# Kernel tuning notes

Hardware: AMD Instinct MI355X
Metric: run time of the kernel (lower is better)

The kernel has to match this reference:

```python
import jax, jax.numpy as jnp
from jax import lax
import numpy as np

K = 48          # dim_embedding_key
PAST = 20
FUT = 40
N = 65536       # total surrounding-agent nodes
E = 1048576     # edges
B = 1           # batch (structurally forced to 1 by the original code)


def conv1d_relu(x, w, b):
    # x: [B, 2, T], w: [K, 2, 3], padding=1 -> relu(Conv1d)
    y = lax.conv_general_dilated(x, w, (1,), ((1, 1),),
                                 dimension_numbers=('NCH', 'OIH', 'NCH'))
    return jax.nn.relu(y + b[None, :, None])


def gru_cell(xt, h, Wih, Whh, bih, bhh):
    gi = xt @ Wih.T + bih
    gh = h @ Whh.T + bhh
    ir, iz, inn = jnp.split(gi, 3, axis=-1)
    hr, hz, hn = jnp.split(gh, 3, axis=-1)
    r = jax.nn.sigmoid(ir + hr)
    z = jax.nn.sigmoid(iz + hz)
    n = jnp.tanh(inn + r * hn)
    return (1 - z) * n + z * h


def gru_last(x, Wih, Whh, bih, bhh):
    # x: [Nb, T, Din]; returns final hidden state [Nb, H] (torch GRU, h0 = 0)
    h0 = jnp.zeros((x.shape[0], Whh.shape[1]), x.dtype)
    def step(h, xt):
        h2 = gru_cell(xt, h, Wih, Whh, bih, bhh)
        return h2, None
    hT, _ = lax.scan(step, h0, jnp.swapaxes(x, 0, 1))
    return hT


def gcn_conv(x, row, col, w, W, b, n):
    # PyG GCNConv(normalize=True): add self loops (weight 1), symmetric norm,
    # x @ W.T, gather at source `row`, scatter-add at target `col`, + bias.
    loop = jnp.arange(n)
    row = jnp.concatenate([row, loop])
    col = jnp.concatenate([col, loop])
    w = jnp.concatenate([w, jnp.ones((n,), w.dtype)])
    deg = jax.ops.segment_sum(w, col, num_segments=n)
    dinv = jnp.where(deg > 0, lax.rsqrt(jnp.where(deg > 0, deg, 1.0)), 0.0)
    norm = dinv[row] * w * dinv[col]
    xw = x @ W.T
    msg = xw[row] * norm[:, None]
    return jax.ops.segment_sum(msg, col, num_segments=n) + b


def forward(past, future, x, edge_index, edge_weight,
            conv_past_w, conv_past_b, conv_fut_w, conv_fut_b,
            enc_past_Wih, enc_past_Whh, enc_past_bih, enc_past_bhh,
            enc_fut_Wih, enc_fut_Whh, enc_fut_bih, enc_fut_bhh,
            dec_Wih, dec_Whh, dec_bih, dec_bhh,
            fc_w, fc_b, gcn1_w, gcn1_b, gcn2_w, gcn2_b):
    present0 = past[:, -1, :2]                                  # [B, 2]

    # --- surrounding agents: conv1d + GRU encoder over all N nodes ---
    inter_past = jnp.swapaxes(x.reshape(-1, PAST, 2), 1, 2)     # [N, 2, T]
    story_embed = jnp.swapaxes(conv1d_relu(inter_past, conv_past_w, conv_past_b), 1, 2)
    state_past = gru_last(story_embed, enc_past_Wih, enc_past_Whh, enc_past_bih, enc_past_bhh)  # [N, K]

    # --- GCN interaction (edge_weight nonempty branch); dropout is eval-mode identity ---
    ei = edge_index.reshape(2, -1)
    ew = edge_weight.reshape(-1)
    x1 = jax.nn.relu(gcn_conv(state_past, ei[0], ei[1], ew, gcn1_w, gcn1_b, N))
    x1 = gcn_conv(x1, ei[0], ei[1], ew, gcn2_w, gcn2_b, N)
    interact_past = x1[0].reshape(B, -1)                        # [B, K] (B == 1)

    # --- ego past / future encoders ---
    past_embed = jnp.swapaxes(conv1d_relu(jnp.swapaxes(past, 1, 2), conv_past_w, conv_past_b), 1, 2)
    fut_embed = jnp.swapaxes(conv1d_relu(jnp.swapaxes(future, 1, 2), conv_fut_w, conv_fut_b), 1, 2)
    target_past = gru_last(past_embed, enc_past_Wih, enc_past_Whh, enc_past_bih, enc_past_bhh)   # [B, K]
    state_fut = gru_last(fut_embed, enc_fut_Wih, enc_fut_Whh, enc_fut_bih, enc_fut_bhh)          # [B, K]

    state_conc = jnp.concatenate([interact_past, target_past, state_fut], axis=-1)               # [B, 3K]

    zeros_in = jnp.zeros_like(state_conc)
    def step(carry, i):
        h, present = carry
        inp = jnp.where(i == 0, state_conc, zeros_in)
        h = gru_cell(inp, h, dec_Wih, dec_Whh, dec_bih, dec_bhh)
        coords = present + h @ fc_w.T + fc_b
        return (h, coords), coords
    (_, _), coords_seq = lax.scan(step, (jnp.zeros((B, 3 * K), past.dtype), present0), jnp.arange(FUT))
    return jnp.swapaxes(coords_seq, 0, 1)                        # [B, FUT, 2]


def setup_inputs() -> dict:
    ks = jax.random.split(jax.random.key(0), 32)
    def p(k, shape, s=0.1):
        return jax.random.normal(k, shape, jnp.float32) * s
    inp = {
        'past': p(ks[0], (B, PAST, 2), 1.0),
        'future': p(ks[1], (B, FUT, 2), 1.0),
        'x': p(ks[2], (N, PAST, 2), 1.0),
        'edge_index': jax.random.randint(ks[3], (1, 2, E), 0, N, jnp.int32),
        'edge_weight': jax.random.uniform(ks[4], (1, E), jnp.float32),
        'conv_past_w': p(ks[5], (K, 2, 3)), 'conv_past_b': p(ks[6], (K,)),
        'conv_fut_w': p(ks[7], (K, 2, 3)), 'conv_fut_b': p(ks[8], (K,)),
        'enc_past_Wih': p(ks[9], (3 * K, K)), 'enc_past_Whh': p(ks[10], (3 * K, K)),
        'enc_past_bih': p(ks[11], (3 * K,)), 'enc_past_bhh': p(ks[12], (3 * K,)),
        'enc_fut_Wih': p(ks[13], (3 * K, K)), 'enc_fut_Whh': p(ks[14], (3 * K, K)),
        'enc_fut_bih': p(ks[15], (3 * K,)), 'enc_fut_bhh': p(ks[16], (3 * K,)),
        'dec_Wih': p(ks[17], (9 * K, 3 * K)), 'dec_Whh': p(ks[18], (9 * K, 3 * K)),
        'dec_bih': p(ks[19], (9 * K,)), 'dec_bhh': p(ks[20], (9 * K,)),
        'fc_w': p(ks[21], (2, 3 * K)), 'fc_b': p(ks[22], (2,)),
        'gcn1_w': p(ks[23], (K, K)), 'gcn1_b': p(ks[24], (K,)),
        'gcn2_w': p(ks[25], (K, K)), 'gcn2_b': p(ks[26], (K,)),
    }
    return inp


def reference(past, future, x, edge_index, edge_weight,
              conv_past_w, conv_past_b, conv_fut_w, conv_fut_b,
              enc_past_Wih, enc_past_Whh, enc_past_bih, enc_past_bhh,
              enc_fut_Wih, enc_fut_Whh, enc_fut_bih, enc_fut_bhh,
              dec_Wih, dec_Whh, dec_bih, dec_bhh,
              fc_w, fc_b, gcn1_w, gcn1_b, gcn2_w, gcn2_b):
    return forward(past, future, x, edge_index, edge_weight,
                   conv_past_w, conv_past_b, conv_fut_w, conv_fut_b,
                   enc_past_Wih, enc_past_Whh, enc_past_bih, enc_past_bhh,
                   enc_fut_Wih, enc_fut_Whh, enc_fut_bih, enc_fut_bhh,
                   dec_Wih, dec_Whh, dec_bih, dec_bhh,
                   fc_w, fc_b, gcn1_w, gcn1_b, gcn2_w, gcn2_b)
```

## Files before the change

kernel.cpp:

```cpp
#include <hip/hip_runtime.h>
#include <math.h>

#define NN 65536
#define NE 1048576
#define KH 48
#define G3 144
#define DEGB 512

#define CAP_L1 8192
#define CAP_S1 4096
#define CAP_E2 65536
#define CAP_S2 8192

#define OFF_MARK1  0u
#define OFF_MARK2  262144u
#define OFF_CNT    524288u
#define OFF_L1R    524352u
#define OFF_L1W    557120u
#define OFF_S1G    589888u
#define OFF_E2R    606272u
#define OFF_E2S    868416u
#define OFF_E2W    1130560u
#define OFF_S2     1392704u
#define OFF_DEG2   1425472u
#define OFF_STATE  1458240u
#define OFF_X1     3031104u
#define OFF_TPSF   3817536u
#define OFF_WHH16  3818048u
#define OFF_GI0P   3942464u

typedef _Float16 h2_t __attribute__((ext_vector_type(2)));
typedef _Float16 h4_t __attribute__((ext_vector_type(4)));

__device__ __forceinline__ float sigmf(float x) { return 1.0f / (1.0f + expf(-x)); }

#if __has_builtin(__builtin_amdgcn_fdot2)
__device__ __forceinline__ float fdot2f(h2_t a, h2_t b, float c) {
    return __builtin_amdgcn_fdot2(a, b, c, false);
}
#else
__device__ __forceinline__ float fdot2f(h2_t a, h2_t b, float c) {
    return c + (float)a.x * (float)b.x + (float)a.y * (float)b.y;
}
#endif

__global__ void k_edges1(const int* ei, const float* ew,
                         int* mark1, unsigned* cnt, int* l1r, float* l1w) {
    int q = blockIdx.x * blockDim.x + threadIdx.x;
    if (q >= NE / 4) return;
    if (q == 0) mark1[0] = 1;
    int4 c4 = reinterpret_cast<const int4*>(ei + NE)[q];
    int e = q * 4;
    int cc[4] = {c4.x, c4.y, c4.z, c4.w};
#pragma unroll
    for (int j = 0; j < 4; ++j) {
        if (cc[j] == 0) {
            int r = ei[e + j];
            float w = ew[e + j];
            unsigned s = atomicAdd(&cnt[0], 1u);
            if (s < CAP_L1) { l1r[s] = r; l1w[s] = w; }
            mark1[r] = 1;
        }
    }
}

__global__ void k_compact1(int* mark1, int* mark2, unsigned* cnt,
                           int* e2r, int* e2s, float* e2w, int* s1g,
                           float* x1, const float* g1b) {
    int i = blockIdx.x * blockDim.x + threadIdx.x;
    if (i >= NN) return;
    if (mark1[i]) {
        unsigned s = atomicAdd(&cnt[1], 1u);
        if (s < CAP_S1) {
            mark1[i] = (int)s + 1;
            mark2[i] = 1;
            s1g[s] = i;
            unsigned t = atomicAdd(&cnt[2], 1u);
            if (t < CAP_E2) { e2r[t] = i; e2s[t] = (int)s; e2w[t] = 1.0f; }
            for (int k = 0; k < KH; ++k) x1[s * KH + k] = g1b[k];
        } else {
            mark1[i] = 0;
        }
    }
}

__global__ void k_edges2(const int* ei, const float* ew,
                         const int* mark1, int* mark2, unsigned* cnt,
                         int* e2r, int* e2s, float* e2w) {
    int q = blockIdx.x * blockDim.x + threadIdx.x;
    if (q >= NE / 4) return;
    int4 c4 = reinterpret_cast<const int4*>(ei + NE)[q];
    int e = q * 4;
    int cc[4] = {c4.x, c4.y, c4.z, c4.w};
#pragma unroll
    for (int j = 0; j < 4; ++j) {
        int m = mark1[cc[j]];
        if (m > 0) {
            int r = ei[e + j];
            float w = ew[e + j];
            unsigned s = atomicAdd(&cnt[2], 1u);
            if (s < CAP_E2) { e2r[s] = r; e2s[s] = m - 1; e2w[s] = w; }
            mark2[r] = 1;
        }
    }
}

__global__ void k_compact2(int* mark2, unsigned* cnt, int* s2, float* deg2) {
    int i = blockIdx.x * blockDim.x + threadIdx.x;
    if (i >= NN) return;
    if (mark2[i]) {
        unsigned s = atomicAdd(&cnt[3], 1u);
        if (s < CAP_S2) { s2[s] = i; mark2[i] = (int)s + 1; deg2[s] = 1.0f; }
        else mark2[i] = 0;
    }
}

__device__ void gru_seq(const float* xseq, int T,
                        const float* cw, const float* cb,
                        const float* Wih, const float* Whh,
                        const float* bih, const float* bhh,
                        float* out48,
                        float* s_x, float* s_embed, float* s_giA,
                        float* s_h, float* s_gh) {
    int t = threadIdx.x;
    int nt = blockDim.x;
    for (int i = t; i < T * 2; i += nt) s_x[i] = xseq[i];
    __syncthreads();
    for (int idx = t; idx < T * KH; idx += nt) {
        int tt = idx / KH;
        int k = idx - tt * KH;
        float acc = cb[k];
#pragma unroll
        for (int d = 0; d < 3; ++d) {
            int tau = tt + d - 1;
            if (tau >= 0 && tau < T) {
                acc += cw[k * 6 + d] * s_x[tau * 2 + 0];
                acc += cw[k * 6 + 3 + d] * s_x[tau * 2 + 1];
            }
        }
        s_embed[tt * KH + k] = fmaxf(acc, 0.0f);
    }
    __syncthreads();
    for (int idx = t; idx < T * G3; idx += nt) {
        int step = idx / G3;
        int row = idx - step * G3;
        const float4* wp = reinterpret_cast<const float4*>(Wih + row * KH);
        const float4* em = reinterpret_cast<const float4*>(s_embed + step * KH);
        float g = bih[row];
#pragma unroll
        for (int j = 0; j < 12; ++j) {
            float4 w4 = wp[j]; float4 e4 = em[j];
            g += w4.x * e4.x + w4.y * e4.y + w4.z * e4.z + w4.w * e4.w;
        }
        s_giA[idx] = g;
    }
    float4 wh[12];
    float bh = 0.0f;
    if (t < G3) {
        const float4* q = reinterpret_cast<const float4*>(Whh + t * KH);
#pragma unroll
        for (int j = 0; j < 12; ++j) wh[j] = q[j];
        bh = bhh[t];
    }
    if (t < KH) s_h[t] = 0.0f;
    __syncthreads();
    for (int step = 0; step < T; ++step) {
        if (t < G3) {
            const float4* hp = reinterpret_cast<const float4*>(s_h);
            float g = bh;
#pragma unroll
            for (int j = 0; j < 12; ++j) {
                float4 h4 = hp[j];
                g += wh[j].x * h4.x + wh[j].y * h4.y + wh[j].z * h4.z + wh[j].w * h4.w;
            }
            s_gh[t] = g;
        }
        __syncthreads();
        if (t < KH) {
            const float* gi = s_giA + step * G3;
            float r = sigmf(gi[t] + s_gh[t]);
            float z = sigmf(gi[KH + t] + s_gh[KH + t]);
            float n = tanhf(gi[2 * KH + t] + r * s_gh[2 * KH + t]);
            s_h[t] = (1.0f - z) * n + z * s_h[t];
        }
        __syncthreads();
    }
    if (t < KH) out48[t] = s_h[t];
}

__global__ __launch_bounds__(192, 2) void k_gru(
    const float* x, const float* cpw, const float* cpb,
    const float* epWih, const float* epWhh, const float* epbih, const float* epbhh,
    const float* cfw, const float* cfb,
    const float* efWih, const float* efWhh, const float* efbih, const float* efbhh,
    const float* past, const float* future,
    const int* ei, const float* ew, const int* mark2, float* deg2,
    const int* s2, const unsigned* cnt, float* state, float* tpsf) {
    if (blockIdx.x < DEGB) {
        int per = NE / DEGB;
        int lo = blockIdx.x * per;
        for (int e = lo + threadIdx.x; e < lo + per; e += blockDim.x) {
            int c = ei[NE + e];
            int m = mark2[c];
            if (m > 0) atomicAdd(&deg2[m - 1], ew[e]);
        }
        return;
    }
    __shared__ __align__(16) float s_x[80];
    __shared__ __align__(16) float s_embed[40 * KH];
    __shared__ __align__(16) float s_giA[40 * G3];
    __shared__ __align__(16) float s_h[KH];
    __shared__ float s_gh[G3];
    if (blockIdx.x == DEGB) {
        gru_seq(past, 20, cpw, cpb, epWih, epWhh, epbih, epbhh,
                tpsf, s_x, s_embed, s_giA, s_h, s_gh);
        return;
    }
    if (blockIdx.x == DEGB + 1) {
        gru_seq(future, 40, cfw, cfb, efWih, efWhh, efbih, efbhh,
                tpsf + 64, s_x, s_embed, s_giA, s_h, s_gh);
        return;
    }
    int b0 = blockIdx.x - (DEGB + 2);
    int nw = gridDim.x - (DEGB + 2);
    int cnt2 = (int)min(cnt[3], (unsigned)CAP_S2);
    for (int b = b0; b < cnt2; b += nw) {
        int node = s2[b];
        gru_seq(x + (size_t)node * 40, 20, cpw, cpb, epWih, epWhh, epbih, epbhh,
                state + (size_t)b * KH, s_x, s_embed, s_giA, s_h, s_gh);
    }
}

__global__ void k_stage(const float* dWhh, const float* dWih,
                        const float* dbih, const float* tpsf,
                        _Float16* whh16, float* gi0p) {
    int id = blockIdx.x * blockDim.x + threadIdx.x;
    if (id < 27 * 576) {
        int c = id / 576, t = id - c * 576;
        int k = t >> 2, q = t & 3;
        int g = c / 9, u = c - g * 9;
        const float* src = dWhh + (size_t)(g * G3 + k) * G3 + q * 36 + 4 * u;
        float4 f = *reinterpret_cast<const float4*>(src);
        h2_t a, b;
        a.x = (_Float16)f.x; a.y = (_Float16)f.y;
        b.x = (_Float16)f.z; b.y = (_Float16)f.w;
        h2_t* o = reinterpret_cast<h2_t*>(whh16);
        o[2 * id + 0] = a;
        o[2 * id + 1] = b;
        return;
    }
    int row = id - 27 * 576;
    if (row < 432) {
        const float* wr = dWih + (size_t)row * G3;
        float acc = dbih[row];
#pragma unroll
        for (int m = 0; m < 48; ++m) acc += wr[48 + m] * tpsf[m];
#pragma unroll
        for (int m = 0; m < 48; ++m) acc += wr[96 + m] * tpsf[64 + m];
        gi0p[row] = acc;
    }
}

__global__ void k_acc1(const unsigned* cnt, const int* e2r, const int* e2s,
                       const float* e2w, const int* mark2, const float* deg2,
                       const int* s1g, const float* state,
                       const float* W1, float* x1) {
    int nE = (int)min(cnt[2], (unsigned)CAP_E2);
    int total = nE * KH;
    int stride = gridDim.x * blockDim.x;
    for (int idx = blockIdx.x * blockDim.x + threadIdx.x; idx < total; idx += stride) {
        int e = idx / KH;
        int k = idx - e * KH;
        int row = e2r[e];
        int s2i = mark2[row] - 1;
        if (s2i < 0) continue;
        int cglob = s1g[e2s[e]];
        int cs2 = mark2[cglob] - 1;
        float norm = e2w[e] * rsqrtf(deg2[s2i] * deg2[cs2]);
        const float* sp = state + (size_t)s2i * KH;
        const float* wp = W1 + k * KH;
        float acc = 0.0f;
#pragma unroll
        for (int m = 0; m < KH; ++m) acc += sp[m] * wp[m];
        atomicAdd(&x1[e2s[e] * KH + k], acc * norm);
    }
}

__global__ __launch_bounds__(640, 1) void k_dec(
    const unsigned* cnt, const int* l1r, const float* l1w,
    const int* mark1, const int* mark2, const float* deg2, const float* x1,
    const float* W2, const float* b2, const float* tpsf, const float* past,
    const float* dWih, const _Float16* whh16, const float* gi0p,
    const float* dbih, const float* dbhh,
    const float* fcw, const float* fcb, float* out) {
    __shared__ __align__(16) float s_conc[G3];
    __shared__ __align__(16) _Float16 s_h16[2][G3];
    __shared__ __align__(16) float s_hf[2][G3];
    int t = threadIdx.x;
    if (t < 48) s_conc[t] = b2[t];
    else if (t < 96) s_conc[t] = tpsf[t - 48];
    else if (t < 144) s_conc[t] = tpsf[64 + t - 96];
    if (t < G3) {
        s_h16[0][t] = (_Float16)0.0f;
        s_hf[0][t] = 0.0f;
    }
    __syncthreads();
    int cl1 = (int)min(cnt[0], (unsigned)CAP_L1);
    float dinv0 = rsqrtf(deg2[mark2[0] - 1]);
    int items = (cl1 + 1) * KH;
    for (int idx = t; idx < items; idx += blockDim.x) {
        int e = idx / KH;
        int k = idx - e * KH;
        int row; float norm;
        if (e == cl1) { row = 0; norm = dinv0 * dinv0; }
        else {
            row = l1r[e];
            int rs2 = mark2[row] - 1;
            if (rs2 < 0) continue;
            norm = l1w[e] * rsqrtf(deg2[rs2]) * dinv0;
        }
        int s1 = mark1[row] - 1;
        if (s1 < 0) continue;
        const float* xp = x1 + (size_t)s1 * KH;
        const float* wp = W2 + k * KH;
        float acc = 0.0f;
#pragma unroll
        for (int m = 0; m < KH; ++m) acc += fmaxf(xp[m], 0.0f) * wp[m];
        atomicAdd(&s_conc[k], acc * norm);
    }
    int k = t >> 2, q = t & 3;
    h2_t wh[54];
    float bh[3] = {0.0f, 0.0f, 0.0f};
    float bi[3] = {0.0f, 0.0f, 0.0f};
    if (t < 576) {
        const h4_t* wp = reinterpret_cast<const h4_t*>(whh16);
#pragma unroll
        for (int c = 0; c < 27; ++c) {
            h4_t v = wp[c * 576 + t];
            wh[2 * c] = __builtin_shufflevector(v, v, 0, 1);
            wh[2 * c + 1] = __builtin_shufflevector(v, v, 2, 3);
        }
        if (q == 0) {
#pragma unroll
            for (int g = 0; g < 3; ++g) {
                bh[g] = dbhh[g * G3 + k];
                bi[g] = dbih[g * G3 + k];
            }
        }
    }
    float fw0[3] = {0, 0, 0}, fw1[3] = {0, 0, 0};
    float fcb0 = 0.0f, fcb1 = 0.0f, pres0 = 0.0f, pres1 = 0.0f;
    if (t >= 576) {
        int lane = t - 576;
#pragma unroll
        for (int j = 0; j < 3; ++j) {
            int m = lane + 64 * j;
            if (m < G3) { fw0[j] = fcw[m]; fw1[j] = fcw[G3 + m]; }
        }
        if (lane == 0) {
            fcb0 = fcb[0]; fcb1 = fcb[1];
            pres0 = past[38]; pres1 = past[39];
        }
    }
    __syncthreads();
    float gi0[3] = {0.0f, 0.0f, 0.0f};
    if (t < 576) {
#pragma unroll
        for (int g = 0; g < 3; ++g) {
            float acc = 0.0f;
            if (q == 0) {
                const float4* p = reinterpret_cast<const float4*>(
                    dWih + (size_t)(g * G3 + k) * G3);
                const float4* cc = reinterpret_cast<const float4*>(s_conc);
#pragma unroll
                for (int j = 0; j < 9; ++j) {
                    float4 w4 = p[j]; float4 c4 = cc[j];
                    acc += w4.x * c4.x + w4.y * c4.y + w4.z * c4.z + w4.w * c4.w;
                }
            } else if (q == 1) {
                const float4* p = reinterpret_cast<const float4*>(
                    dWih + (size_t)(g * G3 + k) * G3 + 36);
                const float4* cc = reinterpret_cast<const float4*>(s_conc + 36);
#pragma unroll
                for (int j = 0; j < 3; ++j) {
                    float4 w4 = p[j]; float4 c4 = cc[j];
                    acc += w4.x * c4.x + w4.y * c4.y + w4.z * c4.z + w4.w * c4.w;
                }
            }
            acc += __shfl_xor(acc, 1);
            acc += __shfl_xor(acc, 2);
            gi0[g] = acc + gi0p[g * G3 + k];
        }
    }
    float hk = 0.0f;
    for (int i = 0; i < 40; ++i) {
        __syncthreads();
        int cur = i & 1, nxt = cur ^ 1;
        if (t < 576) {
            const h4_t* hp = reinterpret_cast<const h4_t*>(&s_h16[cur][0]) + q * 9;
            float a0 = bh[0], a1 = bh[1], a2 = bh[2];
#pragma unroll
            for (int j = 0; j < 9; ++j) {
                h4_t hv = hp[j];
                h2_t lo = __builtin_shufflevector(hv, hv, 0, 1);
                h2_t hi = __builtin_shufflevector(hv, hv, 2, 3);
                a0 = fdot2f(wh[2 * j], lo, a0);
                a1 = fdot2f(wh[18 + 2 * j], lo, a1);
                a2 = fdot2f(wh[36 + 2 * j], lo, a2);
                a0 = fdot2f(wh[2 * j + 1], hi, a0);
                a1 = fdot2f(wh[18 + 2 * j + 1], hi, a1);
                a2 = fdot2f(wh[36 + 2 * j + 1], hi, a2);
            }
            a0 += __shfl_xor(a0, 1); a0 += __shfl_xor(a0, 2);
            a1 += __shfl_xor(a1, 1); a1 += __shfl_xor(a1, 2);
            a2 += __shfl_xor(a2, 1); a2 += __shfl_xor(a2, 2);
            if (q == 0) {
                float gr = ((i == 0) ? gi0[0] : bi[0]) + a0;
                float gz = ((i == 0) ? gi0[1] : bi[1]) + a1;
                float gn = ((i == 0) ? gi0[2] : bi[2]);
                float r = sigmf(gr);
                float z = sigmf(gz);
                float n = tanhf(gn + r * a2);
                hk = (1.0f - z) * n + z * hk;
                s_h16[nxt][k] = (_Float16)hk;
                s_hf[nxt][k] = hk;
            }
        } else if (i >= 1) {
            int lane = t - 576;
            const float* hsrc = s_hf[cur];
            float p0 = 0.0f, p1 = 0.0f;
#pragma unroll
            for (int j = 0; j < 3; ++j) {
                int m = lane + 64 * j;
                if (m < G3) { float h = hsrc[m]; p0 += h * fw0[j]; p1 += h * fw1[j]; }
            }
#pragma unroll
            for (int off = 32; off > 0; off >>= 1) {
                p0 += __shfl_down(p0, off);
                p1 += __shfl_down(p1, off);
            }
            if (lane == 0) {
                pres0 += p0 + fcb0; pres1 += p1 + fcb1;
                out[(i - 1) * 2 + 0] = pres0;
                out[(i - 1) * 2 + 1] = pres1;
            }
        }
    }
    __syncthreads();
    if (t >= 576) {
        int lane = t - 576;
        const float* hsrc = s_hf[0];
        float p0 = 0.0f, p1 = 0.0f;
#pragma unroll
        for (int j = 0; j < 3; ++j) {
            int m = lane + 64 * j;
            if (m < G3) { float h = hsrc[m]; p0 += h * fw0[j]; p1 += h * fw1[j]; }
        }
#pragma unroll
        for (int off = 32; off > 0; off >>= 1) {
            p0 += __shfl_down(p0, off);
            p1 += __shfl_down(p1, off);
        }
        if (lane == 0) {
            pres0 += p0 + fcb0; pres1 += p1 + fcb1;
            out[39 * 2 + 0] = pres0;
            out[39 * 2 + 1] = pres1;
        }
    }
}

extern "C" void kernel_launch(void* const* d_in, const int* in_sizes, int n_in,
                              void* d_out, int out_size, void* d_ws, size_t ws_size,
                              hipStream_t stream) {
    (void)in_sizes; (void)n_in; (void)out_size; (void)ws_size;
    const float* past   = (const float*)d_in[0];
    const float* future = (const float*)d_in[1];
    const float* x      = (const float*)d_in[2];
    const int*   ei     = (const int*)d_in[3];
    const float* ew     = (const float*)d_in[4];
    const float* cpw    = (const float*)d_in[5];
    const float* cpb    = (const float*)d_in[6];
    const float* cfw    = (const float*)d_in[7];
    const float* cfb    = (const float*)d_in[8];
    const float* epWih  = (const float*)d_in[9];
    const float* epWhh  = (const float*)d_in[10];
    const float* epbih  = (const float*)d_in[11];
    const float* epbhh  = (const float*)d_in[12];
    const float* efWih  = (const float*)d_in[13];
    const float* efWhh  = (const float*)d_in[14];
    const float* efbih  = (const float*)d_in[15];
    const float* efbhh  = (const float*)d_in[16];
    const float* dWih   = (const float*)d_in[17];
    const float* dWhh   = (const float*)d_in[18];
    const float* dbih   = (const float*)d_in[19];
    const float* dbhh   = (const float*)d_in[20];
    const float* fcw    = (const float*)d_in[21];
    const float* fcb    = (const float*)d_in[22];
    const float* g1w    = (const float*)d_in[23];
    const float* g1b    = (const float*)d_in[24];
    const float* g2w    = (const float*)d_in[25];
    const float* g2b    = (const float*)d_in[26];

    char* ws = (char*)d_ws;
    int*      mark1 = (int*)(ws + OFF_MARK1);
    int*      mark2 = (int*)(ws + OFF_MARK2);
    unsigned* cnt   = (unsigned*)(ws + OFF_CNT);
    int*      l1r   = (int*)(ws + OFF_L1R);
    float*    l1w   = (float*)(ws + OFF_L1W);
    int*      s1g   = (int*)(ws + OFF_S1G);
    int*      e2r   = (int*)(ws + OFF_E2R);
    int*      e2s   = (int*)(ws + OFF_E2S);
    float*    e2w   = (float*)(ws + OFF_E2W);
    int*      s2    = (int*)(ws + OFF_S2);
    float*    deg2  = (float*)(ws + OFF_DEG2);
    float*    state = (float*)(ws + OFF_STATE);
    float*    x1    = (float*)(ws + OFF_X1);
    float*    tpsf  = (float*)(ws + OFF_TPSF);
    _Float16* whh16 = (_Float16*)(ws + OFF_WHH16);
    float*    gi0p  = (float*)(ws + OFF_GI0P);

    hipMemsetAsync(ws, 0, 524352, stream);
    k_edges1<<<NE / 4 / 256, 256, 0, stream>>>(ei, ew, mark1, cnt, l1r, l1w);
    k_compact1<<<NN / 256, 256, 0, stream>>>(mark1, mark2, cnt, e2r, e2s, e2w, s1g, x1, g1b);
    k_edges2<<<NE / 4 / 256, 256, 0, stream>>>(ei, ew, mark1, mark2, cnt, e2r, e2s, e2w);
    k_compact2<<<NN / 256, 256, 0, stream>>>(mark2, cnt, s2, deg2);
    k_gru<<<DEGB + 2 + 512, 192, 0, stream>>>(x, cpw, cpb, epWih, epWhh, epbih, epbhh,
                                              cfw, cfb, efWih, efWhh, efbih, efbhh,
                                              past, future, ei, ew, mark2, deg2,
                                              s2, cnt, state, tpsf);
    k_stage<<<63, 256, 0, stream>>>(dWhh, dWih, dbih, tpsf, whh16, gi0p);
    k_acc1<<<128, 256, 0, stream>>>(cnt, e2r, e2s, e2w, mark2, deg2, s1g, state, g1w, x1);
    k_dec<<<1, 640, 0, stream>>>(cnt, l1r, l1w, mark1, mark2, deg2, x1, g2w, g2b,
                                 tpsf, past, dWih, whh16, gi0p, dbih, dbhh, fcw, fcb,
                                 (float*)d_out);
}
```

Before: 244.8 us.

## Fuse GRU gate compute with update using pair shuffles; merge staging into acc1

The GRU recurrence now gives each hidden unit a pair of threads that compute all three gate dot products over half of h each. The halves are combined with a lane shuffle and the same thread applies the gate update directly, using a double-buffered shared hidden state. This removes one barrier per step and the s_gh shared round trip, at the cost of 18 float4 registers of weights per thread. Separately, the k_stage kernel is folded into k_acc1 as 64 extra blocks, saving one kernel launch.

```diff
diff --git a/kernel.cpp b/kernel.cpp
--- a/kernel.cpp
+++ b/kernel.cpp
@@ -121,7 +121,7 @@
                         const float* bih, const float* bhh,
                         float* out48,
                         float* s_x, float* s_embed, float* s_giA,
-                        float* s_h, float* s_gh) {
+                        float* s_h ) {
     int t = threadIdx.x;
     int nt = blockDim.x;
     for (int i = t; i < T * 2; i += nt) s_x[i] = xseq[i];
@@ -154,38 +154,51 @@
         }
         s_giA[idx] = g;
     }
-    float4 wh[12];
-    float bh = 0.0f;
-    if (t < G3) {
-        const float4* q = reinterpret_cast<const float4*>(Whh + t * KH);
-#pragma unroll
-        for (int j = 0; j < 12; ++j) wh[j] = q[j];
-        bh = bhh[t];
+    int k = t >> 1, hf = t & 1;
+    float4 wr[18];
+    float bh0 = 0.0f, bh1 = 0.0f, bh2 = 0.0f;
+    if (t < 96) {
+#pragma unroll
+        for (int g = 0; g < 3; ++g) {
+            const float4* q = reinterpret_cast<const float4*>(
+                Whh + (g * KH + k) * KH + hf * 24);
+#pragma unroll
+            for (int j = 0; j < 6; ++j) wr[g * 6 + j] = q[j];
+        }
+        if (hf == 0) { bh0 = bhh[k]; bh1 = bhh[KH + k]; bh2 = bhh[2 * KH + k]; }
     }
     if (t < KH) s_h[t] = 0.0f;
+    float hk = 0.0f;
+    for (int step = 0; step < T; ++step) {
+        __syncthreads();
+        int cur = step & 1, nxt = cur ^ 1;
+        if (t < 96) {
+            const float4* hp = reinterpret_cast<const float4*>(s_h + cur * KH)
+                               + hf * 6;
+            float a0 = bh0, a1 = bh1, a2 = bh2;
+#pragma unroll
+            for (int j = 0; j < 6; ++j) {
+                float4 hv = hp[j];
+                float4 w0 = wr[j], w1 = wr[6 + j], w2 = wr[12 + j];
+                a0 += w0.x * hv.x + w0.y * hv.y + w0.z * hv.z + w0.w * hv.w;
+                a1 += w1.x * hv.x + w1.y * hv.y + w1.z * hv.z + w1.w * hv.w;
+                a2 += w2.x * hv.x + w2.y * hv.y + w2.z * hv.z + w2.w * hv.w;
+            }
+            a0 += __shfl_xor(a0, 1);
+            a1 += __shfl_xor(a1, 1);
+            a2 += __shfl_xor(a2, 1);
+            if (hf == 0) {
+                const float* gi = s_giA + step * G3;
+                float r = sigmf(gi[k] + a0);
+                float z = sigmf(gi[KH + k] + a1);
+                float n = tanhf(gi[2 * KH + k] + r * a2);
+                hk = (1.0f - z) * n + z * hk;
+                s_h[nxt * KH + k] = hk;
+            }
+        }
+    }
     __syncthreads();
-    for (int step = 0; step < T; ++step) {
-        if (t < G3) {
-            const float4* hp = reinterpret_cast<const float4*>(s_h);
-            float g = bh;
-#pragma unroll
-            for (int j = 0; j < 12; ++j) {
-                float4 h4 = hp[j];
-                g += wh[j].x * h4.x + wh[j].y * h4.y + wh[j].z * h4.z + wh[j].w * h4.w;
-            }
-            s_gh[t] = g;
-        }
-        __syncthreads();
-        if (t < KH) {
-            const float* gi = s_giA + step * G3;
-            float r = sigmf(gi[t] + s_gh[t]);
-            float z = sigmf(gi[KH + t] + s_gh[KH + t]);
-            float n = tanhf(gi[2 * KH + t] + r * s_gh[2 * KH + t]);
-            s_h[t] = (1.0f - z) * n + z * s_h[t];
-        }
-        __syncthreads();
-    }
-    if (t < KH) out48[t] = s_h[t];
+    if (t < KH) out48[t] = s_h[(T & 1) * KH + t];
 }
 
 __global__ __launch_bounds__(192, 2) void k_gru(
@@ -209,16 +222,15 @@
     __shared__ __align__(16) float s_x[80];
     __shared__ __align__(16) float s_embed[40 * KH];
     __shared__ __align__(16) float s_giA[40 * G3];
-    __shared__ __align__(16) float s_h[KH];
-    __shared__ float s_gh[G3];
+    __shared__ __align__(16) float s_h[2 * KH];
     if (blockIdx.x == DEGB) {
         gru_seq(past, 20, cpw, cpb, epWih, epWhh, epbih, epbhh,
-                tpsf, s_x, s_embed, s_giA, s_h, s_gh);
+                tpsf, s_x, s_embed, s_giA, s_h);
         return;
     }
     if (blockIdx.x == DEGB + 1) {
         gru_seq(future, 40, cfw, cfb, efWih, efWhh, efbih, efbhh,
-                tpsf + 64, s_x, s_embed, s_giA, s_h, s_gh);
+                tpsf + 64, s_x, s_embed, s_giA, s_h);
         return;
     }
     int b0 = blockIdx.x - (DEGB + 2);
@@ -227,48 +239,50 @@
     for (int b = b0; b < cnt2; b += nw) {
         int node = s2[b];
         gru_seq(x + (size_t)node * 40, 20, cpw, cpb, epWih, epWhh, epbih, epbhh,
-                state + (size_t)b * KH, s_x, s_embed, s_giA, s_h, s_gh);
-    }
-}
-
-__global__ void k_stage(const float* dWhh, const float* dWih,
-                        const float* dbih, const float* tpsf,
-                        _Float16* whh16, float* gi0p) {
-    int id = blockIdx.x * blockDim.x + threadIdx.x;
-    if (id < 27 * 576) {
-        int c = id / 576, t = id - c * 576;
-        int k = t >> 2, q = t & 3;
-        int g = c / 9, u = c - g * 9;
-        const float* src = dWhh + (size_t)(g * G3 + k) * G3 + q * 36 + 4 * u;
-        float4 f = *reinterpret_cast<const float4*>(src);
-        h2_t a, b;
-        a.x = (_Float16)f.x; a.y = (_Float16)f.y;
-        b.x = (_Float16)f.z; b.y = (_Float16)f.w;
-        h2_t* o = reinterpret_cast<h2_t*>(whh16);
-        o[2 * id + 0] = a;
-        o[2 * id + 1] = b;
-        return;
-    }
-    int row = id - 27 * 576;
-    if (row < 432) {
-        const float* wr = dWih + (size_t)row * G3;
-        float acc = dbih[row];
-#pragma unroll
-        for (int m = 0; m < 48; ++m) acc += wr[48 + m] * tpsf[m];
-#pragma unroll
-        for (int m = 0; m < 48; ++m) acc += wr[96 + m] * tpsf[64 + m];
-        gi0p[row] = acc;
+                state + (size_t)b * KH, s_x, s_embed, s_giA, s_h);
     }
 }
 
 __global__ void k_acc1(const unsigned* cnt, const int* e2r, const int* e2s,
                        const float* e2w, const int* mark2, const float* deg2,
                        const int* s1g, const float* state,
-                       const float* W1, float* x1) {
+                       const float* W1, float* x1,
+                       const float* dWhh, const float* dWih,
+                       const float* dbih, const float* tpsf,
+                       _Float16* whh16, float* gi0p) {
+    if (blockIdx.x < 64) {
+        int id = blockIdx.x * blockDim.x + threadIdx.x;
+        if (id < 27 * 576) {
+            int c = id / 576, t = id - c * 576;
+            int k = t >> 2, q = t & 3;
+            int g = c / 9, u = c - g * 9;
+            const float* src = dWhh + (size_t)(g * G3 + k) * G3 + q * 36 + 4 * u;
+            float4 f = *reinterpret_cast<const float4*>(src);
+            h2_t a, b;
+            a.x = (_Float16)f.x; a.y = (_Float16)f.y;
+            b.x = (_Float16)f.z; b.y = (_Float16)f.w;
+            h2_t* o = reinterpret_cast<h2_t*>(whh16);
+            o[2 * id + 0] = a;
+            o[2 * id + 1] = b;
+            return;
+        }
+        int row = id - 27 * 576;
+        if (row < 432) {
+            const float* wr = dWih + (size_t)row * G3;
+            float acc = dbih[row];
+#pragma unroll
+            for (int m = 0; m < 48; ++m) acc += wr[48 + m] * tpsf[m];
+#pragma unroll
+            for (int m = 0; m < 48; ++m) acc += wr[96 + m] * tpsf[64 + m];
+            gi0p[row] = acc;
+        }
+        return;
+    }
     int nE = (int)min(cnt[2], (unsigned)CAP_E2);
     int total = nE * KH;
-    int stride = gridDim.x * blockDim.x;
-    for (int idx = blockIdx.x * blockDim.x + threadIdx.x; idx < total; idx += stride) {
+    int stride = (gridDim.x - 64) * blockDim.x;
+    for (int idx = (blockIdx.x - 64) * blockDim.x + threadIdx.x; idx < total;
+         idx += stride) {
         int e = idx / KH;
         int k = idx - e * KH;
         int row = e2r[e];
@@ -528,8 +542,9 @@
                                               cfw, cfb, efWih, efWhh, efbih, efbhh,
                                               past, future, ei, ew, mark2, deg2,
                                               s2, cnt, state, tpsf);
-    k_stage<<<63, 256, 0, stream>>>(dWhh, dWih, dbih, tpsf, whh16, gi0p);
-    k_acc1<<<128, 256, 0, stream>>>(cnt, e2r, e2s, e2w, mark2, deg2, s1g, state, g1w, x1);
+    k_acc1<<<64 + 128, 256, 0, stream>>>(cnt, e2r, e2s, e2w, mark2, deg2, s1g,
+                                         state, g1w, x1,
+                                         dWhh, dWih, dbih, tpsf, whh16, gi0p);
     k_dec<<<1, 640, 0, stream>>>(cnt, l1r, l1w, mark1, mark2, deg2, x1, g2w, g2b,
                                  tpsf, past, dWih, whh16, gi0p, dbih, dbhh, fcw, fcb,
                                  (float*)d_out);
```

Measured after the change: 241.9 us. No clear change (-1.2%).
